# Performance work log

Hardware: AMD Instinct MI355X
Metric: run time of the kernel (lower is better)

The kernel has to match this reference:

```python
import jax, jax.numpy as jnp
import numpy as np

B, H, S, D = 2, 16, 2048, 128  # batch, heads, seq_len, head_dim (hidden=2048, heads=16)


def setup_inputs() -> dict:
    key = jax.random.key(0)
    kq, kk, kv = jax.random.split(key, 3)
    q = jax.random.normal(kq, (B, H, S, D), dtype=jnp.float32)
    k = jax.random.normal(kk, (B, H, S, D), dtype=jnp.float32)
    v = jax.random.normal(kv, (B, H, S, D), dtype=jnp.float32)
    return {"q": q, "k": k, "v": v}


def reference(q, k, v):
    # scores = (q @ k^T) / sqrt(head_dim)  -> [B, H, S, S]
    scaling = 1.0 / jnp.sqrt(jnp.asarray(q.shape[-1], dtype=q.dtype))
    scores = jnp.einsum('bhqd,bhkd->bhqk', q, k) * scaling
    # softmax over keys (dropout p=0.0 -> identity in eval / p=0)
    weights = jax.nn.softmax(scores, axis=-1)
    # out = weights @ v -> [B, H, S, D]
    return jnp.einsum('bhqk,bhkd->bhqd', weights, v)
```

## Files before the change

### kernel.cpp

```cpp
#include <hip/hip_runtime.h>
#include <stdint.h>

typedef __attribute__((ext_vector_type(4))) float f32x4;
typedef __attribute__((ext_vector_type(16))) float f32x16;
typedef __attribute__((ext_vector_type(8))) short bf16x8;

constexpr int S_ = 2048;
constexpr int D_ = 128;
constexpr int BH = 32;
constexpr int KB = 64;
constexpr int NT = S_ / KB;
constexpr float QSCALE = 0.08838834764831845f * 1.4426950408889634f;

__device__ __forceinline__ short f2bf(float f) {
  uint32_t u = __float_as_uint(f);
  u += 0x7fffu + ((u >> 16) & 1u);
  return (short)(u >> 16);
}

__global__ void prep_kf(const float* __restrict__ k, short* __restrict__ kf) {
  __shared__ short Lt[32][132];
  const int bh = blockIdx.x >> 6;
  const int c = blockIdx.x & 63;
  const int t = threadIdx.x;
#pragma unroll
  for (int i = 0; i < 4; ++i) {
    int g = t + 256 * i;
    int r = g >> 5, c4 = g & 31;
    float4 f = reinterpret_cast<const float4*>(k)[((size_t)bh * S_ + c * 32 + r) * 32 + c4];
    short* d = &Lt[r][c4 * 4];
    d[0] = f2bf(f.x); d[1] = f2bf(f.y); d[2] = f2bf(f.z); d[3] = f2bf(f.w);
  }
  __syncthreads();
#pragma unroll
  for (int i = 0; i < 2; ++i) {
    int gw = t + 256 * i;
    int s = gw >> 6, lane = gw & 63;
    int l32 = lane & 31, hi = lane >> 5;
    bf16x8 o;
#pragma unroll
    for (int j = 0; j < 8; ++j) o[j] = Lt[l32][s * 16 + hi * 8 + j];
    *reinterpret_cast<bf16x8*>(
        &kf[((size_t)(bh * 64 + c) * 8 + s) * 512 + lane * 8]) = o;
  }
}

__global__ void prep_vf(const float* __restrict__ v, short* __restrict__ vf) {
  __shared__ short Lt[64][132];
  const int bh = blockIdx.x >> 5;
  const int tt = blockIdx.x & 31;
  const int t = threadIdx.x;
#pragma unroll
  for (int i = 0; i < 8; ++i) {
    int g = t + 256 * i;
    int r = g >> 5, c4 = g & 31;
    float4 f = reinterpret_cast<const float4*>(v)[((size_t)bh * S_ + tt * 64 + r) * 32 + c4];
    short* d = &Lt[r][c4 * 4];
    d[0] = f2bf(f.x); d[1] = f2bf(f.y); d[2] = f2bf(f.z); d[3] = f2bf(f.w);
  }
  __syncthreads();
#pragma unroll
  for (int i = 0; i < 4; ++i) {
    int gw = t + 256 * i;
    int f = gw >> 6, lane = gw & 63;
    int ks2 = f >> 2, d0 = f & 3;
    int l32 = lane & 31, hi = lane >> 5;
    bf16x8 o;
#pragma unroll
    for (int j = 0; j < 8; ++j) o[j] = Lt[(ks2 * 2 + hi) * 8 + j][d0 * 32 + l32];
    *reinterpret_cast<bf16x8*>(
        &vf[((size_t)(bh * 32 + tt) * 16 + f) * 512 + lane * 8]) = o;
  }
}

__global__ __launch_bounds__(256, 2) void attn_fwd_v12(
    const float* __restrict__ q, const short* __restrict__ kf,
    const short* __restrict__ vf, float* __restrict__ out)
{
  const int lid = blockIdx.x;
  const int swz = (lid & 7) * 64 + (lid >> 3);
  const int qt = swz & 15;
  const int bh = swz >> 4;

  const int tid = threadIdx.x;
  const int wid = tid >> 6;
  const int lane = tid & 63;
  const int l32 = lane & 31;
  const int hi = lane >> 5;

  const int qrow = qt * 128 + wid * 32 + l32;

  bf16x8 bq[8];
  {
    const float* qg_ = q + ((size_t)bh * S_ + qrow) * D_ + hi * 8;
#pragma unroll
    for (int s = 0; s < 8; ++s) {
      float4 f0 = *reinterpret_cast<const float4*>(qg_ + s * 16);
      float4 f1 = *reinterpret_cast<const float4*>(qg_ + s * 16 + 4);
      bf16x8 a;
      a[0] = f2bf(f0.x * QSCALE); a[1] = f2bf(f0.y * QSCALE);
      a[2] = f2bf(f0.z * QSCALE); a[3] = f2bf(f0.w * QSCALE);
      a[4] = f2bf(f1.x * QSCALE); a[5] = f2bf(f1.y * QSCALE);
      a[6] = f2bf(f1.z * QSCALE); a[7] = f2bf(f1.w * QSCALE);
      bq[s] = a;
    }
  }

  const short* kbase = kf + (size_t)bh * 64 * 8 * 512 + lane * 8;
  const short* vbase = vf + (size_t)bh * 32 * 16 * 512 + lane * 8;

  f32x16 oacc[4], loacc;
#pragma unroll
  for (int d0 = 0; d0 < 4; ++d0)
#pragma unroll
    for (int r = 0; r < 16; ++r) oacc[d0][r] = 0.f;
#pragma unroll
  for (int r = 0; r < 16; ++r) loacc[r] = 0.f;

  union { uint32_t u[4]; bf16x8 b; } onesu;
#pragma unroll
  for (int i = 0; i < 4; ++i) onesu.u[i] = 0x3F803F80u;

  for (int t = 0; t < NT; ++t) {
    const short* kt = kbase + (size_t)t * 16 * 512;
    const short* vt_ = vbase + (size_t)t * 16 * 512;

    bf16x8 kreg[16];
#pragma unroll
    for (int g = 0; g < 16; ++g)
      kreg[g] = *reinterpret_cast<const bf16x8*>(kt + g * 512);

    f32x16 sf0, sf1;
#pragma unroll
    for (int r = 0; r < 16; ++r) { sf0[r] = 0.f; sf1[r] = 0.f; }
    __builtin_amdgcn_s_setprio(1);
#pragma unroll
    for (int s = 0; s < 8; ++s) {
      sf0 = __builtin_amdgcn_mfma_f32_32x32x16_bf16(kreg[s], bq[s], sf0, 0, 0, 0);
      sf1 = __builtin_amdgcn_mfma_f32_32x32x16_bf16(kreg[8 + s], bq[s], sf1, 0, 0, 0);
    }
    __builtin_amdgcn_s_setprio(0);

    bf16x8 vreg[16];
#pragma unroll
    for (int f = 0; f < 16; ++f)
      vreg[f] = *reinterpret_cast<const bf16x8*>(vt_ + f * 512);

    bf16x8 pfrag[4];
#define MAKE_P(SF, F0)                                                          \
    {                                                                           \
      uint32_t w[8];                                                            \
      _Pragma("unroll")                                                         \
      for (int i2 = 0; i2 < 8; ++i2) {                                          \
        float e0 = exp2f(SF[2 * i2]);                                           \
        float e1 = exp2f(SF[2 * i2 + 1]);                                       \
        asm("v_cvt_pk_bf16_f32 %0, %1, %2" : "=v"(w[i2]) : "v"(e0), "v"(e1));   \
      }                                                                         \
      asm("v_permlane32_swap_b32 %0, %1" : "+v"(w[0]), "+v"(w[2]));             \
      asm("v_permlane32_swap_b32 %0, %1" : "+v"(w[1]), "+v"(w[3]));             \
      asm("v_permlane32_swap_b32 %0, %1" : "+v"(w[4]), "+v"(w[6]));             \
      asm("v_permlane32_swap_b32 %0, %1" : "+v"(w[5]), "+v"(w[7]));             \
      union { int4 i4; bf16x8 b; } u0, u1;                                      \
      u0.i4 = (int4){(int)w[0], (int)w[1], (int)w[2], (int)w[3]};               \
      u1.i4 = (int4){(int)w[4], (int)w[5], (int)w[6], (int)w[7]};               \
      pfrag[F0] = u0.b; pfrag[F0 + 1] = u1.b;                                   \
    }
    MAKE_P(sf0, 0)
    MAKE_P(sf1, 2)
#undef MAKE_P

    __builtin_amdgcn_s_setprio(1);
#pragma unroll
    for (int ks2 = 0; ks2 < 4; ++ks2) {
#pragma unroll
      for (int d0 = 0; d0 < 4; ++d0)
        oacc[d0] = __builtin_amdgcn_mfma_f32_32x32x16_bf16(
            vreg[ks2 * 4 + d0], pfrag[ks2], oacc[d0], 0, 0, 0);
      loacc = __builtin_amdgcn_mfma_f32_32x32x16_bf16(onesu.b, pfrag[ks2], loacc, 0, 0, 0);
    }
    __builtin_amdgcn_s_setprio(0);
  }

  const float inv = 1.0f / loacc[0];
  float* ob = out + ((size_t)bh * S_ + qrow) * D_;
#pragma unroll
  for (int d0 = 0; d0 < 4; ++d0)
#pragma unroll
    for (int r2 = 0; r2 < 4; ++r2) {
      float4 o4 = {oacc[d0][r2 * 4 + 0] * inv, oacc[d0][r2 * 4 + 1] * inv,
                   oacc[d0][r2 * 4 + 2] * inv, oacc[d0][r2 * 4 + 3] * inv};
      *reinterpret_cast<float4*>(ob + d0 * 32 + r2 * 8 + hi * 4) = o4;
    }
}

__global__ __launch_bounds__(256, 4) void attn_fwd_v1(
    const float* __restrict__ q, const float* __restrict__ k,
    const float* __restrict__ v, float* __restrict__ out)
{
  __shared__ __align__(16) short Klds[32 * 128];
  __shared__ __align__(16) short Vlds[128 * 40];
  __shared__ __align__(16) short Plds[4][16 * 40];
  const int lid = blockIdx.x;
  const int swz = (lid & 7) * 128 + (lid >> 3);
  const int qt = swz & 31;
  const int bh = swz >> 5;
  const int tid = threadIdx.x;
  const int wid = tid >> 6;
  const int lane = tid & 63;
  const int l16 = lane & 15;
  const int lhi = lane >> 4;
  const int qrow0 = qt * 64 + wid * 16;
  const float* qg = q + ((size_t)bh * S_ + qrow0 + l16) * D_;
  const float* kg = k + (size_t)bh * S_ * D_;
  const float* vg = v + (size_t)bh * S_ * D_;
  bf16x8 aq[4];
#pragma unroll
  for (int ks = 0; ks < 4; ++ks) {
    const float* p = qg + ks * 32 + lhi * 8;
    float4 f0 = *reinterpret_cast<const float4*>(p);
    float4 f1 = *reinterpret_cast<const float4*>(p + 4);
    bf16x8 a;
    a[0] = f2bf(f0.x * QSCALE); a[1] = f2bf(f0.y * QSCALE);
    a[2] = f2bf(f0.z * QSCALE); a[3] = f2bf(f0.w * QSCALE);
    a[4] = f2bf(f1.x * QSCALE); a[5] = f2bf(f1.y * QSCALE);
    a[6] = f2bf(f1.z * QSCALE); a[7] = f2bf(f1.w * QSCALE);
    aq[ks] = a;
  }
  float mrow[4], lrow[4];
  f32x4 oacc[8];
#pragma unroll
  for (int r = 0; r < 4; ++r) { mrow[r] = -1e30f; lrow[r] = 0.f; }
#pragma unroll
  for (int i = 0; i < 8; ++i) oacc[i] = (f32x4){0.f, 0.f, 0.f, 0.f};
  for (int t = 0; t < S_ / 32; ++t) {
    const int kv0 = t * 32;
    __syncthreads();
#pragma unroll
    for (int i = 0; i < 2; ++i) {
      const int g = tid * 2 + i;
      const int row = g >> 4;
      const int c8 = g & 15;
      const float* ksrc = kg + (size_t)(kv0 + row) * D_ + c8 * 8;
      float4 f0 = *reinterpret_cast<const float4*>(ksrc);
      float4 f1 = *reinterpret_cast<const float4*>(ksrc + 4);
      bf16x8 kk;
      kk[0] = f2bf(f0.x); kk[1] = f2bf(f0.y); kk[2] = f2bf(f0.z); kk[3] = f2bf(f0.w);
      kk[4] = f2bf(f1.x); kk[5] = f2bf(f1.y); kk[6] = f2bf(f1.z); kk[7] = f2bf(f1.w);
      *reinterpret_cast<bf16x8*>(
          &Klds[row * D_ + ((c8 * 8) ^ ((row & 7) << 3))]) = kk;
      const float* vsrc = vg + (size_t)(kv0 + row) * D_ + c8 * 8;
      float4 g0 = *reinterpret_cast<const float4*>(vsrc);
      float4 g1 = *reinterpret_cast<const float4*>(vsrc + 4);
      const int dbase = c8 * 8;
      Vlds[(dbase + 0) * 40 + row] = f2bf(g0.x);
      Vlds[(dbase + 1) * 40 + row] = f2bf(g0.y);
      Vlds[(dbase + 2) * 40 + row] = f2bf(g0.z);
      Vlds[(dbase + 3) * 40 + row] = f2bf(g0.w);
      Vlds[(dbase + 4) * 40 + row] = f2bf(g1.x);
      Vlds[(dbase + 5) * 40 + row] = f2bf(g1.y);
      Vlds[(dbase + 6) * 40 + row] = f2bf(g1.z);
      Vlds[(dbase + 7) * 40 + row] = f2bf(g1.w);
    }
    __syncthreads();
    f32x4 sfrag[2];
#pragma unroll
    for (int kb = 0; kb < 2; ++kb) {
      f32x4 acc = (f32x4){0.f, 0.f, 0.f, 0.f};
#pragma unroll
      for (int ks = 0; ks < 4; ++ks) {
        const int rowk = kb * 16 + l16;
        bf16x8 bk = *reinterpret_cast<const bf16x8*>(
            &Klds[rowk * D_ + (((ks * 4 + lhi) * 8) ^ ((rowk & 7) << 3))]);
        acc = __builtin_amdgcn_mfma_f32_16x16x32_bf16(aq[ks], bk, acc, 0, 0, 0);
      }
      sfrag[kb] = acc;
    }
    float mt[4];
#pragma unroll
    for (int r = 0; r < 4; ++r) mt[r] = fmaxf(sfrag[0][r], sfrag[1][r]);
#pragma unroll
    for (int off = 1; off < 16; off <<= 1)
#pragma unroll
      for (int r = 0; r < 4; ++r) mt[r] = fmaxf(mt[r], __shfl_xor(mt[r], off, 64));
    float al[4], ps[4];
#pragma unroll
    for (int r = 0; r < 4; ++r) {
      float mn = fmaxf(mrow[r], mt[r]);
      al[r] = exp2f(mrow[r] - mn);
      mrow[r] = mn;
      ps[r] = 0.f;
    }
#pragma unroll
    for (int kb = 0; kb < 2; ++kb)
#pragma unroll
      for (int r = 0; r < 4; ++r) {
        float p = exp2f(sfrag[kb][r] - mrow[r]);
        ps[r] += p;
        Plds[wid][(lhi * 4 + r) * 40 + kb * 16 + l16] = f2bf(p);
      }
#pragma unroll
    for (int off = 1; off < 16; off <<= 1)
#pragma unroll
      for (int r = 0; r < 4; ++r) ps[r] += __shfl_xor(ps[r], off, 64);
#pragma unroll
    for (int r = 0; r < 4; ++r) lrow[r] = lrow[r] * al[r] + ps[r];
#pragma unroll
    for (int i = 0; i < 8; ++i)
#pragma unroll
      for (int r = 0; r < 4; ++r) oacc[i][r] *= al[r];
    bf16x8 ap = *reinterpret_cast<const bf16x8*>(&Plds[wid][l16 * 40 + lhi * 8]);
#pragma unroll
    for (int d0 = 0; d0 < 8; ++d0) {
      bf16x8 bv = *reinterpret_cast<const bf16x8*>(
          &Vlds[(d0 * 16 + l16) * 40 + lhi * 8]);
      oacc[d0] = __builtin_amdgcn_mfma_f32_16x16x32_bf16(ap, bv, oacc[d0], 0, 0, 0);
    }
  }
#pragma unroll
  for (int r = 0; r < 4; ++r) {
    float inv = 1.0f / lrow[r];
    float* orow = out + ((size_t)bh * S_ + qrow0 + lhi * 4 + r) * D_ + l16;
#pragma unroll
    for (int d0 = 0; d0 < 8; ++d0) orow[d0 * 16] = oacc[d0][r] * inv;
  }
}

extern "C" void kernel_launch(void* const* d_in, const int* in_sizes, int n_in,
                              void* d_out, int out_size, void* d_ws, size_t ws_size,
                              hipStream_t stream) {
  (void)in_sizes; (void)n_in; (void)out_size;
  const float* q = (const float*)d_in[0];
  const float* k = (const float*)d_in[1];
  const float* v = (const float*)d_in[2];
  float* o = (float*)d_out;
  const size_t NEL = (size_t)BH * S_ * D_;
  const size_t need = NEL * 2 * sizeof(short);
  if (ws_size >= need) {
    short* kfb = (short*)d_ws;
    short* vfb = kfb + NEL;
    hipLaunchKernelGGL(prep_kf, dim3(2048), dim3(256), 0, stream, k, kfb);
    hipLaunchKernelGGL(prep_vf, dim3(1024), dim3(256), 0, stream, v, vfb);
    hipLaunchKernelGGL(attn_fwd_v12, dim3(512), dim3(256), 0, stream, q, kfb, vfb, o);
  } else {
    hipLaunchKernelGGL(attn_fwd_v1, dim3(1024), dim3(256), 0, stream, q, k, v, o);
  }
}
```

Baseline: 116.2 us.

## Stage K tiles through triple-buffered LDS with async global-to-LDS loads

K is now converted to plain row-major bf16 and each block loads shared K tiles into a three-slot LDS ring using global_load_lds, prefetching the next tile while computing the current one. Before, every wave read its own swizzled K fragments straight from global memory. The row-sum MFMA against a ones vector is replaced by a scalar running sum plus a final cross-half shuffle. V loads and the P@V MFMAs are split into two halves so the softmax exponentials for the second half overlap with MFMAs of the first. The cost is added barriers and LDS usage, and the LDS reads of K may hit bank conflicts.

Result: faster. 109.6 us (-5.8%).

```diff
diff --git a/kernel.cpp b/kernel.cpp
--- a/kernel.cpp
+++ b/kernel.cpp
@@ -18,30 +18,23 @@
   return (short)(u >> 16);
 }
 
-__global__ void prep_kf(const float* __restrict__ k, short* __restrict__ kf) {
-  __shared__ short Lt[32][132];
-  const int bh = blockIdx.x >> 6;
-  const int c = blockIdx.x & 63;
-  const int t = threadIdx.x;
-#pragma unroll
-  for (int i = 0; i < 4; ++i) {
-    int g = t + 256 * i;
-    int r = g >> 5, c4 = g & 31;
-    float4 f = reinterpret_cast<const float4*>(k)[((size_t)bh * S_ + c * 32 + r) * 32 + c4];
-    short* d = &Lt[r][c4 * 4];
-    d[0] = f2bf(f.x); d[1] = f2bf(f.y); d[2] = f2bf(f.z); d[3] = f2bf(f.w);
-  }
-  __syncthreads();
-#pragma unroll
-  for (int i = 0; i < 2; ++i) {
-    int gw = t + 256 * i;
-    int s = gw >> 6, lane = gw & 63;
-    int l32 = lane & 31, hi = lane >> 5;
+__device__ __forceinline__ void gll16(const void* g, void* l) {
+  __builtin_amdgcn_global_load_lds(
+      (const __attribute__((address_space(1))) void*)g,
+      (__attribute__((address_space(3))) void*)l, 16, 0, 0);
+}
+
+__global__ void prep_k(const float* __restrict__ k, short* __restrict__ kb) {
+  const size_t N8 = (size_t)BH * S_ * D_ / 8;
+  size_t i = (size_t)blockIdx.x * blockDim.x + threadIdx.x;
+  const size_t stride = (size_t)gridDim.x * blockDim.x;
+  for (; i < N8; i += stride) {
+    float4 a = reinterpret_cast<const float4*>(k)[i * 2];
+    float4 b = reinterpret_cast<const float4*>(k)[i * 2 + 1];
     bf16x8 o;
-#pragma unroll
-    for (int j = 0; j < 8; ++j) o[j] = Lt[l32][s * 16 + hi * 8 + j];
-    *reinterpret_cast<bf16x8*>(
-        &kf[((size_t)(bh * 64 + c) * 8 + s) * 512 + lane * 8]) = o;
+    o[0] = f2bf(a.x); o[1] = f2bf(a.y); o[2] = f2bf(a.z); o[3] = f2bf(a.w);
+    o[4] = f2bf(b.x); o[5] = f2bf(b.y); o[6] = f2bf(b.z); o[7] = f2bf(b.w);
+    reinterpret_cast<bf16x8*>(kb)[i] = o;
   }
 }
 
@@ -73,10 +66,12 @@
   }
 }
 
-__global__ __launch_bounds__(256, 2) void attn_fwd_v12(
-    const float* __restrict__ q, const short* __restrict__ kf,
+__global__ __launch_bounds__(256, 2) void attn_fwd_v13(
+    const float* __restrict__ q, const short* __restrict__ kbf,
     const short* __restrict__ vf, float* __restrict__ out)
 {
+  __shared__ __align__(16) short Klds[3][8192];
+
   const int lid = blockIdx.x;
   const int swz = (lid & 7) * 64 + (lid >> 3);
   const int qt = swz & 15;
@@ -106,29 +101,47 @@
     }
   }
 
-  const short* kbase = kf + (size_t)bh * 64 * 8 * 512 + lane * 8;
+  const short* kg = kbf + (size_t)bh * S_ * D_;
   const short* vbase = vf + (size_t)bh * 32 * 16 * 512 + lane * 8;
 
-  f32x16 oacc[4], loacc;
+  int kofs[4];
+#pragma unroll
+  for (int j = 0; j < 4; ++j) kofs[j] = lane * D_ + (wid * 4 + j) * 8;
+  auto stage = [&](int t) {
+    const short* ks = kg + (size_t)(t * KB) * D_;
+    short* kd = &Klds[t % 3][(wid * 4) * 512];
+#pragma unroll
+    for (int j = 0; j < 4; ++j) gll16(ks + kofs[j], kd + j * 512);
+  };
+
+  f32x16 oacc[4];
 #pragma unroll
   for (int d0 = 0; d0 < 4; ++d0)
 #pragma unroll
     for (int r = 0; r < 16; ++r) oacc[d0][r] = 0.f;
-#pragma unroll
-  for (int r = 0; r < 16; ++r) loacc[r] = 0.f;
-
-  union { uint32_t u[4]; bf16x8 b; } onesu;
-#pragma unroll
-  for (int i = 0; i < 4; ++i) onesu.u[i] = 0x3F803F80u;
-
+  float lsum = 0.f;
+
+  stage(0);
   for (int t = 0; t < NT; ++t) {
-    const short* kt = kbase + (size_t)t * 16 * 512;
+    if (t + 1 < NT) {
+      stage(t + 1);
+      __builtin_amdgcn_sched_barrier(0);
+      asm volatile("s_waitcnt vmcnt(4)" ::: "memory");
+    } else {
+      __builtin_amdgcn_sched_barrier(0);
+      asm volatile("s_waitcnt vmcnt(0)" ::: "memory");
+    }
+    __builtin_amdgcn_sched_barrier(0);
+    __builtin_amdgcn_s_barrier();
+    __builtin_amdgcn_sched_barrier(0);
+
+    const short* Kb = &Klds[t % 3][0];
     const short* vt_ = vbase + (size_t)t * 16 * 512;
 
-    bf16x8 kreg[16];
-#pragma unroll
-    for (int g = 0; g < 16; ++g)
-      kreg[g] = *reinterpret_cast<const bf16x8*>(kt + g * 512);
+    bf16x8 vregA[8];
+#pragma unroll
+    for (int f = 0; f < 8; ++f)
+      vregA[f] = *reinterpret_cast<const bf16x8*>(vt_ + f * 512);
 
     f32x16 sf0, sf1;
 #pragma unroll
@@ -136,15 +149,17 @@
     __builtin_amdgcn_s_setprio(1);
 #pragma unroll
     for (int s = 0; s < 8; ++s) {
-      sf0 = __builtin_amdgcn_mfma_f32_32x32x16_bf16(kreg[s], bq[s], sf0, 0, 0, 0);
-      sf1 = __builtin_amdgcn_mfma_f32_32x32x16_bf16(kreg[8 + s], bq[s], sf1, 0, 0, 0);
+      bf16x8 a0 = *reinterpret_cast<const bf16x8*>(&Kb[((s * 2 + hi) * 64 + l32) * 8]);
+      bf16x8 a1 = *reinterpret_cast<const bf16x8*>(&Kb[((s * 2 + hi) * 64 + 32 + l32) * 8]);
+      sf0 = __builtin_amdgcn_mfma_f32_32x32x16_bf16(a0, bq[s], sf0, 0, 0, 0);
+      sf1 = __builtin_amdgcn_mfma_f32_32x32x16_bf16(a1, bq[s], sf1, 0, 0, 0);
     }
     __builtin_amdgcn_s_setprio(0);
 
-    bf16x8 vreg[16];
-#pragma unroll
-    for (int f = 0; f < 16; ++f)
-      vreg[f] = *reinterpret_cast<const bf16x8*>(vt_ + f * 512);
+    bf16x8 vregB[8];
+#pragma unroll
+    for (int f = 0; f < 8; ++f)
+      vregB[f] = *reinterpret_cast<const bf16x8*>(vt_ + (8 + f) * 512);
 
     bf16x8 pfrag[4];
 #define MAKE_P(SF, F0)                                                          \
@@ -154,6 +169,7 @@
       for (int i2 = 0; i2 < 8; ++i2) {                                          \
         float e0 = exp2f(SF[2 * i2]);                                           \
         float e1 = exp2f(SF[2 * i2 + 1]);                                       \
+        lsum += e0 + e1;                                                        \
         asm("v_cvt_pk_bf16_f32 %0, %1, %2" : "=v"(w[i2]) : "v"(e0), "v"(e1));   \
       }                                                                         \
       asm("v_permlane32_swap_b32 %0, %1" : "+v"(w[0]), "+v"(w[2]));             \
@@ -166,22 +182,28 @@
       pfrag[F0] = u0.b; pfrag[F0 + 1] = u1.b;                                   \
     }
     MAKE_P(sf0, 0)
-    MAKE_P(sf1, 2)
-#undef MAKE_P
-
     __builtin_amdgcn_s_setprio(1);
 #pragma unroll
-    for (int ks2 = 0; ks2 < 4; ++ks2) {
+    for (int ks2 = 0; ks2 < 2; ++ks2)
 #pragma unroll
       for (int d0 = 0; d0 < 4; ++d0)
         oacc[d0] = __builtin_amdgcn_mfma_f32_32x32x16_bf16(
-            vreg[ks2 * 4 + d0], pfrag[ks2], oacc[d0], 0, 0, 0);
-      loacc = __builtin_amdgcn_mfma_f32_32x32x16_bf16(onesu.b, pfrag[ks2], loacc, 0, 0, 0);
-    }
+            vregA[ks2 * 4 + d0], pfrag[ks2], oacc[d0], 0, 0, 0);
     __builtin_amdgcn_s_setprio(0);
-  }
-
-  const float inv = 1.0f / loacc[0];
+    MAKE_P(sf1, 2)
+    __builtin_amdgcn_s_setprio(1);
+#pragma unroll
+    for (int ks2 = 0; ks2 < 2; ++ks2)
+#pragma unroll
+      for (int d0 = 0; d0 < 4; ++d0)
+        oacc[d0] = __builtin_amdgcn_mfma_f32_32x32x16_bf16(
+            vregB[ks2 * 4 + d0], pfrag[2 + ks2], oacc[d0], 0, 0, 0);
+    __builtin_amdgcn_s_setprio(0);
+#undef MAKE_P
+  }
+
+  lsum += __shfl_xor(lsum, 32, 64);
+  const float inv = 1.0f / lsum;
   float* ob = out + ((size_t)bh * S_ + qrow) * D_;
 #pragma unroll
   for (int d0 = 0; d0 < 4; ++d0)
@@ -336,11 +358,11 @@
   const size_t NEL = (size_t)BH * S_ * D_;
   const size_t need = NEL * 2 * sizeof(short);
   if (ws_size >= need) {
-    short* kfb = (short*)d_ws;
-    short* vfb = kfb + NEL;
-    hipLaunchKernelGGL(prep_kf, dim3(2048), dim3(256), 0, stream, k, kfb);
+    short* kb = (short*)d_ws;
+    short* vfb = kb + NEL;
+    hipLaunchKernelGGL(prep_k, dim3(2048), dim3(256), 0, stream, k, kb);
     hipLaunchKernelGGL(prep_vf, dim3(1024), dim3(256), 0, stream, v, vfb);
-    hipLaunchKernelGGL(attn_fwd_v12, dim3(512), dim3(256), 0, stream, q, kfb, vfb, o);
+    hipLaunchKernelGGL(attn_fwd_v13, dim3(512), dim3(256), 0, stream, q, kb, vfb, o);
   } else {
     hipLaunchKernelGGL(attn_fwd_v1, dim3(1024), dim3(256), 0, stream, q, k, v, o);
   }
```
